# Optimization experiments

Hardware: AMD Instinct MI355X
Metric: run time of the kernel (lower is better)

Reference implementation:

```python
import jax, jax.numpy as jnp
import numpy as np

# dims: M=MC samples, B=graphs, K=latent, H=decoder hidden, N=max nodes, P=permutations
M, B, K, H, N, F_DIM, P = 4, 256, 64, 1024, 50, 3, 64
E = N * (N - 1) // 2  # reduced adjacency = strictly lower triangle
COEFF_A = 1.0
BETA = 1.0
TRIL_I, TRIL_J = np.tril_indices(N, -1)


def setup_inputs() -> dict:
    key = jax.random.key(0)
    ks = jax.random.split(key, 12)
    mean = 0.5 * jax.random.normal(ks[0], (B, K), dtype=jnp.float32)
    logvar = 0.1 * jax.random.normal(ks[1], (B, K), dtype=jnp.float32)
    eps = jax.random.normal(ks[2], (M, B, K), dtype=jnp.float32)
    W1 = jax.random.normal(ks[3], (K, H), dtype=jnp.float32) / np.sqrt(K)
    b1 = jnp.zeros((H,), jnp.float32)
    WA = jax.random.normal(ks[4], (H, E), dtype=jnp.float32) / np.sqrt(H)
    bA = jnp.zeros((E,), jnp.float32)
    WF = jax.random.normal(ks[5], (H, N * F_DIM), dtype=jnp.float32) / np.sqrt(H)
    bF = jnp.zeros((N * F_DIM,), jnp.float32)
    # symmetric binary adjacency with zero diagonal
    U = jax.random.bernoulli(ks[6], 0.15, (B, N, N)).astype(jnp.float32)
    Au = jnp.triu(U, 1)
    A_in = Au + jnp.swapaxes(Au, -1, -2)
    # two bernoulli attributes + one one-hot-categorical attribute (over nodes)
    fb = jax.random.bernoulli(ks[7], 0.3, (B, N, 2)).astype(jnp.float32)
    idx = jax.random.randint(ks[8], (B,), 0, N)
    oh = jax.nn.one_hot(idx, N, dtype=jnp.float32)  # (B, N)
    Fx = jnp.concatenate([fb, oh[..., None]], axis=-1)  # (B, N, 3)
    coeff_Fx = jnp.ones((F_DIM,), jnp.float32)
    permutations = jax.vmap(lambda k: jax.random.permutation(k, N))(
        jax.random.split(ks[9], P)).astype(jnp.int32)  # (P, N)
    return dict(mean=mean, logvar=logvar, eps=eps, W1=W1, b1=b1, WA=WA, bA=bA,
                WF=WF, bF=bF, A_in=A_in, Fx=Fx, coeff_Fx=coeff_Fx,
                permutations=permutations)


def _bernoulli_logprob(x, logits):
    # sum of elementwise Bernoulli log-prob over last axis
    return jnp.sum(x * jax.nn.log_sigmoid(logits)
                   + (1.0 - x) * jax.nn.log_sigmoid(-logits), axis=-1)


def reference(mean, logvar, eps, W1, b1, WA, bA, WF, bF, A_in, Fx, coeff_Fx,
              permutations):
    # pathwise (reparametrised) latent samples: (M, B, K)
    Z = mean + jnp.exp(0.5 * logvar) * eps
    # MLP decoder
    h = jax.nn.relu(Z @ W1 + b1)                       # (M, B, H)
    logits_A = h @ WA + bA                              # (M, B, E)
    logits_Fx = (h @ WF + bF).reshape(M, B, N, F_DIM)   # (M, B, N, F)
    # permutation-matched adjacency: A_perm[b,p,i,j] = A_in[b, perm[p,i], perm[p,j]]
    A_perm = A_in[:, permutations[:, :, None], permutations[:, None, :]]  # (B,P,N,N)
    A_red = A_perm[..., TRIL_I, TRIL_J].reshape(B * P, E)                 # (B*P, E)
    lA = jnp.repeat(logits_A, P, axis=1)                                  # (M, B*P, E)
    nce_A = _bernoulli_logprob(A_red, lA).mean(axis=0)                    # (B*P,)
    nce_A = nce_A.reshape(B, P).max(axis=1)                               # (B,)
    # attribute log-probs: two bernoulli (sum over nodes), one categorical over nodes
    lp_bern = jnp.sum(
        Fx[..., :2] * jax.nn.log_sigmoid(logits_Fx[..., :2])
        + (1.0 - Fx[..., :2]) * jax.nn.log_sigmoid(-logits_Fx[..., :2]),
        axis=-2)                                                          # (M, B, 2)
    lp_cat = jnp.sum(Fx[..., 2] * jax.nn.log_softmax(logits_Fx[..., 2], axis=-1),
                     axis=-1)                                             # (M, B)
    nce_Fx = jnp.concatenate([lp_bern.mean(0), lp_cat.mean(0)[:, None]], axis=-1)  # (B, F)
    # KL(q(z|x) || N(0, I))
    kld = 0.5 * jnp.sum(jnp.exp(logvar) + mean ** 2 - 1.0 - logvar, axis=-1)  # (B,)
    return COEFF_A * nce_A + nce_Fx @ coeff_Fx - BETA * kld
```

## Files before the change

kernel.cpp:

```cpp
#include <hip/hip_runtime.h>
#include <math.h>

#define MM 4
#define BB 256
#define KK 64
#define HH 1024
#define NN 50
#define EE 1225
#define PP 64
#define CTOT 1375
#define NPAD 1408

typedef short short8 __attribute__((ext_vector_type(8)));
typedef float floatx4 __attribute__((ext_vector_type(4)));
typedef unsigned short ushort;

__device__ __forceinline__ ushort f2bf(float f) {
    union { float f; unsigned u; } v; v.f = f;
    unsigned r = v.u + 0x7fffu + ((v.u >> 16) & 1u);
    return (ushort)(r >> 16);
}

__device__ __forceinline__ float logsigm(float l) {
    return -(fmaxf(l, 0.0f) + log1pf(expf(-fabsf(l))));
}

__device__ __forceinline__ float wsum64(float v) {
    #pragma unroll
    for (int m = 1; m < 64; m <<= 1) v += __shfl_xor(v, m);
    return v;
}
__device__ __forceinline__ float wmax64(float v) {
    #pragma unroll
    for (int m = 1; m < 64; m <<= 1) v = fmaxf(v, __shfl_xor(v, m));
    return v;
}

__global__ __launch_bounds__(256) void kA(const float* __restrict__ mean,
                                          const float* __restrict__ logvar,
                                          const float* __restrict__ eps,
                                          const float* __restrict__ W1,
                                          const float* __restrict__ b1,
                                          const float* __restrict__ WA,
                                          const float* __restrict__ WF,
                                          const float* __restrict__ A,
                                          ushort* __restrict__ hB,
                                          ushort* __restrict__ Wt,
                                          float* __restrict__ Sneg,
                                          int*   __restrict__ edgesG,
                                          int*   __restrict__ cntG,
                                          float* __restrict__ kldG) {
    const int t = threadIdx.x;
    __shared__ float smem[64 * 65];
    __shared__ int cnt;

    if (blockIdx.x < 256) {
        const int b = blockIdx.x;
        float4* z4 = (float4*)smem;
        if (t == 0) cnt = 0;
        if (t < 64) {
            float mv = mean[b * 64 + t];
            float lv = logvar[b * 64 + t];
            float sd = expf(0.5f * lv);
            float4 z;
            z.x = mv + sd * eps[(0 * BB + b) * 64 + t];
            z.y = mv + sd * eps[(1 * BB + b) * 64 + t];
            z.z = mv + sd * eps[(2 * BB + b) * 64 + t];
            z.w = mv + sd * eps[(3 * BB + b) * 64 + t];
            z4[t] = z;
            float term = 0.5f * (expf(lv) + mv * mv - 1.0f - lv);
            term = wsum64(term);
            if (t == 0) kldG[b] = term;
        }
        if (t < 4) Sneg[b * 4 + t] = 0.0f;
        __syncthreads();
        const int j0 = t * 4;
        float acc[4][4] = {};
        #pragma unroll 8
        for (int k = 0; k < 64; k++) {
            float4 w = *(const float4*)&W1[k * HH + j0];
            float4 z = z4[k];
            acc[0][0] += z.x * w.x; acc[0][1] += z.x * w.y; acc[0][2] += z.x * w.z; acc[0][3] += z.x * w.w;
            acc[1][0] += z.y * w.x; acc[1][1] += z.y * w.y; acc[1][2] += z.y * w.z; acc[1][3] += z.y * w.w;
            acc[2][0] += z.z * w.x; acc[2][1] += z.z * w.y; acc[2][2] += z.z * w.z; acc[2][3] += z.z * w.w;
            acc[3][0] += z.w * w.x; acc[3][1] += z.w * w.y; acc[3][2] += z.w * w.z; acc[3][3] += z.w * w.w;
        }
        float4 bb = *(const float4*)&b1[j0];
        #pragma unroll
        for (int m = 0; m < 4; m++) {
            unsigned u0 = ((unsigned)f2bf(fmaxf(acc[m][0] + bb.x, 0.f))) |
                          ((unsigned)f2bf(fmaxf(acc[m][1] + bb.y, 0.f)) << 16);
            unsigned u1 = ((unsigned)f2bf(fmaxf(acc[m][2] + bb.z, 0.f))) |
                          ((unsigned)f2bf(fmaxf(acc[m][3] + bb.w, 0.f)) << 16);
            uint2 u; u.x = u0; u.y = u1;
            *(uint2*)&hB[(b * 4 + m) * HH + j0] = u;
        }
        for (int x = t; x < 2500; x += 256) {
            int i = x / NN, j = x - i * NN;
            if (j < i) {
                float a = A[b * 2500 + x];
                if (a != 0.0f) { int id = atomicAdd(&cnt, 1); edgesG[b * 256 + id] = (i << 8) | j; }
            }
        }
        __syncthreads();
        if (t == 0) cntG[b] = cnt;
    } else {
        const int id = blockIdx.x - 256;
        const int kt = id & 15, nt = id >> 4;
        float* T = smem;
        const int k0 = kt * 64, n0 = nt * 64;
        #pragma unroll
        for (int i = 0; i < 16; i++) {
            int x = i * 256 + t;
            int kk = x >> 6, nn = x & 63;
            int gn = n0 + nn, gk = k0 + kk;
            float v = 0.f;
            if (gn < EE)        v = WA[gk * EE + gn];
            else if (gn < CTOT) v = WF[gk * 150 + (gn - EE)];
            T[kk * 65 + nn] = v;
        }
        __syncthreads();
        #pragma unroll
        for (int i = 0; i < 16; i++) {
            int x = i * 256 + t;
            int nn = x >> 6, kk = x & 63;
            Wt[(n0 + nn) * 1024 + k0 + kk] = f2bf(T[kk * 65 + nn]);
        }
    }
}

__global__ __launch_bounds__(256) void k2(const ushort* __restrict__ hB,
                                          const ushort* __restrict__ Wt,
                                          const float* __restrict__ bA,
                                          const float* __restrict__ bF,
                                          float* __restrict__ Lbar,
                                          float* __restrict__ Sneg,
                                          float* __restrict__ lgF) {
    const int ct = blockIdx.x;
    const int rt = blockIdx.y;
    const int t = threadIdx.x;
    const int w = t >> 6, lane = t & 63;
    const int wm = w >> 1, wn = w & 1;
    const int quad = lane >> 4, l16 = lane & 15;
    __shared__ short As[64][72];
    __shared__ short Bs[64][72];
    floatx4 acc[2][2] = {};
    const int row0 = rt * 64, col0 = ct * 64;

    const int r0 = t >> 3, koA = (t & 7) * 8;
    const int r1 = r0 + 32;
    const ushort* pA0 = hB + (row0 + r0) * 1024 + koA;
    const ushort* pA1 = hB + (row0 + r1) * 1024 + koA;
    const ushort* pB0 = Wt + (col0 + r0) * 1024 + koA;
    const ushort* pB1 = Wt + (col0 + r1) * 1024 + koA;

    short8 ra[2], rb[2];
    ra[0] = *(const short8*)(pA0);
    ra[1] = *(const short8*)(pA1);
    rb[0] = *(const short8*)(pB0);
    rb[1] = *(const short8*)(pB1);

    for (int ch = 0; ch < 16; ch++) {
        __syncthreads();
        *(short8*)&As[r0][koA] = ra[0];
        *(short8*)&As[r1][koA] = ra[1];
        *(short8*)&Bs[r0][koA] = rb[0];
        *(short8*)&Bs[r1][koA] = rb[1];
        __syncthreads();
        if (ch < 15) {
            const int off = (ch + 1) * 64;
            ra[0] = *(const short8*)(pA0 + off);
            ra[1] = *(const short8*)(pA1 + off);
            rb[0] = *(const short8*)(pB0 + off);
            rb[1] = *(const short8*)(pB1 + off);
        }
        #pragma unroll
        for (int kk = 0; kk < 2; kk++) {
            int ko = kk * 32 + quad * 8;
            short8 a0 = *(const short8*)&As[wm * 32 + l16][ko];
            short8 a1 = *(const short8*)&As[wm * 32 + 16 + l16][ko];
            short8 b0 = *(const short8*)&Bs[wn * 32 + l16][ko];
            short8 b1 = *(const short8*)&Bs[wn * 32 + 16 + l16][ko];
            acc[0][0] = __builtin_amdgcn_mfma_f32_16x16x32_bf16(a0, b0, acc[0][0], 0, 0, 0);
            acc[0][1] = __builtin_amdgcn_mfma_f32_16x16x32_bf16(a0, b1, acc[0][1], 0, 0, 0);
            acc[1][0] = __builtin_amdgcn_mfma_f32_16x16x32_bf16(a1, b0, acc[1][0], 0, 0, 0);
            acc[1][1] = __builtin_amdgcn_mfma_f32_16x16x32_bf16(a1, b1, acc[1][1], 0, 0, 0);
        }
    }

    #pragma unroll
    for (int mi = 0; mi < 2; mi++) {
        const int grow = row0 + wm * 32 + mi * 16 + quad * 4;
        const int b = grow >> 2;
        float sn0 = 0.f, sn1 = 0.f, sn2 = 0.f, sn3 = 0.f;
        #pragma unroll
        for (int ni = 0; ni < 2; ni++) {
            int gc = col0 + wn * 32 + ni * 16 + l16;
            floatx4 a = acc[mi][ni];
            if (gc < EE) {
                float bias = bA[gc];
                float l0 = a[0] + bias, l1 = a[1] + bias, l2 = a[2] + bias, l3 = a[3] + bias;
                Lbar[b * EE + gc] = 0.25f * (l0 + l1 + l2 + l3);
                sn0 += logsigm(l0); sn1 += logsigm(l1); sn2 += logsigm(l2); sn3 += logsigm(l3);
            } else if (gc < CTOT) {
                int c2 = gc - EE;
                float bias = bF[c2];
                lgF[(b * 4 + 0) * 150 + c2] = a[0] + bias;
                lgF[(b * 4 + 1) * 150 + c2] = a[1] + bias;
                lgF[(b * 4 + 2) * 150 + c2] = a[2] + bias;
                lgF[(b * 4 + 3) * 150 + c2] = a[3] + bias;
            }
        }
        #pragma unroll
        for (int msk = 1; msk < 16; msk <<= 1) {
            sn0 += __shfl_xor(sn0, msk);
            sn1 += __shfl_xor(sn1, msk);
            sn2 += __shfl_xor(sn2, msk);
            sn3 += __shfl_xor(sn3, msk);
        }
        if (l16 == 0) {
            atomicAdd(&Sneg[b * 4 + 0], sn0);
            atomicAdd(&Sneg[b * 4 + 1], sn1);
            atomicAdd(&Sneg[b * 4 + 2], sn2);
            atomicAdd(&Sneg[b * 4 + 3], sn3);
        }
    }
}

__global__ __launch_bounds__(512) void k4(const float* __restrict__ Fx,
                                          const float* __restrict__ coeff,
                                          const int* __restrict__ perms,
                                          const float* __restrict__ Lbar,
                                          const float* __restrict__ Sneg,
                                          const float* __restrict__ lgF,
                                          const int* __restrict__ edgesG,
                                          const int* __restrict__ cntG,
                                          const float* __restrict__ kldG,
                                          float* __restrict__ out) {
    const int b = blockIdx.x;
    const int t = threadIdx.x;
    const int w = t >> 6, lane = t & 63;
    __shared__ int   ip[PP * NN];
    __shared__ float Lb[EE];
    __shared__ int   edges[256];
    __shared__ float lgfs[600];
    __shared__ float mred[4], wmaxs[8];

    const int ne = cntG[b];
    for (int x = t; x < PP * NN; x += 512) {
        int p = x / NN, i = x - p * NN;
        ip[p * NN + perms[x]] = i;
    }
    for (int x = t; x < EE; x += 512) Lb[x] = Lbar[b * EE + x];
    for (int x = t; x < 600; x += 512) lgfs[x] = lgF[b * 600 + x];
    if (t < ne) edges[t] = edgesG[b * 256 + t];
    __syncthreads();

    if (w < 4) {
        float l0 = 0.f, l1 = 0.f, l2 = -INFINITY, x0 = 0.f, x1 = 0.f, x2 = 0.f;
        bool v = lane < NN;
        if (v) {
            l0 = lgfs[w * 150 + lane * 3 + 0];
            l1 = lgfs[w * 150 + lane * 3 + 1];
            l2 = lgfs[w * 150 + lane * 3 + 2];
            x0 = Fx[b * 150 + lane * 3 + 0];
            x1 = Fx[b * 150 + lane * 3 + 1];
            x2 = Fx[b * 150 + lane * 3 + 2];
        }
        float mx = wmax64(l2);
        float es = v ? expf(l2 - mx) : 0.f;
        es = wsum64(es);
        float lse = mx + logf(es);
        float val = 0.f;
        if (v) {
            val = coeff[0] * (logsigm(l0) + x0 * l0)
                + coeff[1] * (logsigm(l1) + x1 * l1)
                + coeff[2] * (x2 * (l2 - lse));
        }
        val = wsum64(val);
        if (lane == 0) mred[w] = val;
    }
    __syncthreads();

    float lmax = -INFINITY;
    for (int p = w; p < PP; p += 8) {
        const int* ipp = &ip[p * NN];
        float acc = 0.f;
        for (int x = lane; x < ne; x += 64) {
            int ed = edges[x];
            int iu = ipp[ed >> 8], iv = ipp[ed & 255];
            int ii = max(iu, iv), jj = min(iu, iv);
            acc += Lb[ii * (ii - 1) / 2 + jj];
        }
        acc = wsum64(acc);
        lmax = fmaxf(lmax, acc);
    }
    if (lane == 0) wmaxs[w] = lmax;
    __syncthreads();
    if (t == 0) {
        float dmax = wmaxs[0];
        #pragma unroll
        for (int i = 1; i < 8; i++) dmax = fmaxf(dmax, wmaxs[i]);
        float sbar = 0.25f * (Sneg[b * 4 + 0] + Sneg[b * 4 + 1] + Sneg[b * 4 + 2] + Sneg[b * 4 + 3]);
        float fxv  = 0.25f * (mred[0] + mred[1] + mred[2] + mred[3]);
        out[b] = (sbar + dmax) + fxv - kldG[b];
    }
}

extern "C" void kernel_launch(void* const* d_in, const int* in_sizes, int n_in,
                              void* d_out, int out_size, void* d_ws, size_t ws_size,
                              hipStream_t stream) {
    const float* mean   = (const float*)d_in[0];
    const float* logvar = (const float*)d_in[1];
    const float* eps    = (const float*)d_in[2];
    const float* W1     = (const float*)d_in[3];
    const float* b1     = (const float*)d_in[4];
    const float* WA     = (const float*)d_in[5];
    const float* bA     = (const float*)d_in[6];
    const float* WF     = (const float*)d_in[7];
    const float* bF     = (const float*)d_in[8];
    const float* A      = (const float*)d_in[9];
    const float* Fx     = (const float*)d_in[10];
    const float* coeff  = (const float*)d_in[11];
    const int*   perms  = (const int*)d_in[12];
    float* out = (float*)d_out;

    ushort* Wt   = (ushort*)d_ws;
    ushort* hB   = Wt + NPAD * 1024;
    float*  Lbar = (float*)(hB + 1024 * 1024);
    float*  Sneg = Lbar + BB * EE;
    float*  lgF  = Sneg + 1024;
    int*    edgesG = (int*)(lgF + 1024 * 150);
    int*    cntG   = edgesG + 256 * 256;
    float*  kldG   = (float*)(cntG + 256);

    kA<<<dim3(608), dim3(256), 0, stream>>>(mean, logvar, eps, W1, b1, WA, WF, A,
                                            hB, Wt, Sneg, edgesG, cntG, kldG);
    k2<<<dim3(22, 16), dim3(256), 0, stream>>>(hB, Wt, bA, bF, Lbar, Sneg, lgF);
    k4<<<dim3(BB), dim3(512), 0, stream>>>(Fx, coeff, perms, Lbar, Sneg, lgF,
                                           edgesG, cntG, kldG, out);
}
```

Measured before the change: 127.4 us.

## Precompute inverse permutations, use full symmetric logit table, double-buffer GEMM LDS

```diff
diff --git a/kernel.cpp b/kernel.cpp
--- a/kernel.cpp
+++ b/kernel.cpp
@@ -44,12 +44,14 @@
                                           const float* __restrict__ WA,
                                           const float* __restrict__ WF,
                                           const float* __restrict__ A,
+                                          const int*   __restrict__ perms,
                                           ushort* __restrict__ hB,
                                           ushort* __restrict__ Wt,
                                           float* __restrict__ Sneg,
                                           int*   __restrict__ edgesG,
                                           int*   __restrict__ cntG,
-                                          float* __restrict__ kldG) {
+                                          float* __restrict__ kldG,
+                                          int*   __restrict__ ipG) {
     const int t = threadIdx.x;
     __shared__ float smem[64 * 65];
     __shared__ int cnt;
@@ -104,7 +106,7 @@
         }
         __syncthreads();
         if (t == 0) cntG[b] = cnt;
-    } else {
+    } else if (blockIdx.x < 608) {
         const int id = blockIdx.x - 256;
         const int kt = id & 15, nt = id >> 4;
         float* T = smem;
@@ -125,6 +127,12 @@
             int x = i * 256 + t;
             int nn = x >> 6, kk = x & 63;
             Wt[(n0 + nn) * 1024 + k0 + kk] = f2bf(T[kk * 65 + nn]);
+        }
+    } else {
+        const int id = blockIdx.x - 608;
+        for (int x = id * 800 + t; x < (id + 1) * 800; x += 256) {
+            int p = x / NN, i = x - p * NN;
+            ipG[p * 51 + perms[x]] = i;
         }
     }
 }
@@ -142,8 +150,8 @@
     const int w = t >> 6, lane = t & 63;
     const int wm = w >> 1, wn = w & 1;
     const int quad = lane >> 4, l16 = lane & 15;
-    __shared__ short As[64][72];
-    __shared__ short Bs[64][72];
+    __shared__ short As[2][64][72];
+    __shared__ short Bs[2][64][72];
     floatx4 acc[2][2] = {};
     const int row0 = rt * 64, col0 = ct * 64;
 
@@ -154,37 +162,44 @@
     const ushort* pB0 = Wt + (col0 + r0) * 1024 + koA;
     const ushort* pB1 = Wt + (col0 + r1) * 1024 + koA;
 
-    short8 ra[2], rb[2];
-    ra[0] = *(const short8*)(pA0);
-    ra[1] = *(const short8*)(pA1);
-    rb[0] = *(const short8*)(pB0);
-    rb[1] = *(const short8*)(pB1);
-
+    short8 ra0 = *(const short8*)(pA0);
+    short8 ra1 = *(const short8*)(pA1);
+    short8 rb0 = *(const short8*)(pB0);
+    short8 rb1 = *(const short8*)(pB1);
+    *(short8*)&As[0][r0][koA] = ra0;
+    *(short8*)&As[0][r1][koA] = ra1;
+    *(short8*)&Bs[0][r0][koA] = rb0;
+    *(short8*)&Bs[0][r1][koA] = rb1;
+    __syncthreads();
+
+    int cur = 0;
     for (int ch = 0; ch < 16; ch++) {
-        __syncthreads();
-        *(short8*)&As[r0][koA] = ra[0];
-        *(short8*)&As[r1][koA] = ra[1];
-        *(short8*)&Bs[r0][koA] = rb[0];
-        *(short8*)&Bs[r1][koA] = rb[1];
-        __syncthreads();
         if (ch < 15) {
             const int off = (ch + 1) * 64;
-            ra[0] = *(const short8*)(pA0 + off);
-            ra[1] = *(const short8*)(pA1 + off);
-            rb[0] = *(const short8*)(pB0 + off);
-            rb[1] = *(const short8*)(pB1 + off);
+            ra0 = *(const short8*)(pA0 + off);
+            ra1 = *(const short8*)(pA1 + off);
+            rb0 = *(const short8*)(pB0 + off);
+            rb1 = *(const short8*)(pB1 + off);
         }
         #pragma unroll
         for (int kk = 0; kk < 2; kk++) {
             int ko = kk * 32 + quad * 8;
-            short8 a0 = *(const short8*)&As[wm * 32 + l16][ko];
-            short8 a1 = *(const short8*)&As[wm * 32 + 16 + l16][ko];
-            short8 b0 = *(const short8*)&Bs[wn * 32 + l16][ko];
-            short8 b1 = *(const short8*)&Bs[wn * 32 + 16 + l16][ko];
+            short8 a0 = *(const short8*)&As[cur][wm * 32 + l16][ko];
+            short8 a1 = *(const short8*)&As[cur][wm * 32 + 16 + l16][ko];
+            short8 b0 = *(const short8*)&Bs[cur][wn * 32 + l16][ko];
+            short8 b1 = *(const short8*)&Bs[cur][wn * 32 + 16 + l16][ko];
             acc[0][0] = __builtin_amdgcn_mfma_f32_16x16x32_bf16(a0, b0, acc[0][0], 0, 0, 0);
             acc[0][1] = __builtin_amdgcn_mfma_f32_16x16x32_bf16(a0, b1, acc[0][1], 0, 0, 0);
             acc[1][0] = __builtin_amdgcn_mfma_f32_16x16x32_bf16(a1, b0, acc[1][0], 0, 0, 0);
             acc[1][1] = __builtin_amdgcn_mfma_f32_16x16x32_bf16(a1, b1, acc[1][1], 0, 0, 0);
+        }
+        if (ch < 15) {
+            *(short8*)&As[cur ^ 1][r0][koA] = ra0;
+            *(short8*)&As[cur ^ 1][r1][koA] = ra1;
+            *(short8*)&Bs[cur ^ 1][r0][koA] = rb0;
+            *(short8*)&Bs[cur ^ 1][r1][koA] = rb1;
+            __syncthreads();
+            cur ^= 1;
         }
     }
 
@@ -229,7 +244,7 @@
 
 __global__ __launch_bounds__(512) void k4(const float* __restrict__ Fx,
                                           const float* __restrict__ coeff,
-                                          const int* __restrict__ perms,
+                                          const int* __restrict__ ipG,
                                           const float* __restrict__ Lbar,
                                           const float* __restrict__ Sneg,
                                           const float* __restrict__ lgF,
@@ -240,21 +255,38 @@
     const int b = blockIdx.x;
     const int t = threadIdx.x;
     const int w = t >> 6, lane = t & 63;
-    __shared__ int   ip[PP * NN];
-    __shared__ float Lb[EE];
+    __shared__ int   ip[PP * 51];
+    __shared__ float LbF[NN * 51];
     __shared__ int   edges[256];
     __shared__ float lgfs[600];
-    __shared__ float mred[4], wmaxs[8];
+    __shared__ float mred[4];
+    __shared__ float psum[8][64];
 
     const int ne = cntG[b];
-    for (int x = t; x < PP * NN; x += 512) {
-        int p = x / NN, i = x - p * NN;
-        ip[p * NN + perms[x]] = i;
-    }
-    for (int x = t; x < EE; x += 512) Lb[x] = Lbar[b * EE + x];
+    for (int x = t; x < PP * 51; x += 512) ip[x] = ipG[x];
+    for (int x = t; x < 2500; x += 512) {
+        int i = x / NN, j = x - i * NN;
+        if (j < i) {
+            float v = Lbar[b * EE + i * (i - 1) / 2 + j];
+            LbF[i * 51 + j] = v;
+            LbF[j * 51 + i] = v;
+        }
+    }
     for (int x = t; x < 600; x += 512) lgfs[x] = lgF[b * 600 + x];
     if (t < ne) edges[t] = edgesG[b * 256 + t];
     __syncthreads();
+
+    {
+        const int ipB = lane * 51;
+        float acc = 0.f;
+        for (int x = w; x < ne; x += 8) {
+            int ed = edges[x];
+            int iu = ip[ipB + (ed >> 8)];
+            int iv = ip[ipB + (ed & 255)];
+            acc += LbF[iu * 51 + iv];
+        }
+        psum[w][lane] = acc;
+    }
 
     if (w < 4) {
         float l0 = 0.f, l1 = 0.f, l2 = -INFINITY, x0 = 0.f, x1 = 0.f, x2 = 0.f;
@@ -282,28 +314,16 @@
     }
     __syncthreads();
 
-    float lmax = -INFINITY;
-    for (int p = w; p < PP; p += 8) {
-        const int* ipp = &ip[p * NN];
-        float acc = 0.f;
-        for (int x = lane; x < ne; x += 64) {
-            int ed = edges[x];
-            int iu = ipp[ed >> 8], iv = ipp[ed & 255];
-            int ii = max(iu, iv), jj = min(iu, iv);
-            acc += Lb[ii * (ii - 1) / 2 + jj];
-        }
-        acc = wsum64(acc);
-        lmax = fmaxf(lmax, acc);
-    }
-    if (lane == 0) wmaxs[w] = lmax;
-    __syncthreads();
-    if (t == 0) {
-        float dmax = wmaxs[0];
-        #pragma unroll
-        for (int i = 1; i < 8; i++) dmax = fmaxf(dmax, wmaxs[i]);
-        float sbar = 0.25f * (Sneg[b * 4 + 0] + Sneg[b * 4 + 1] + Sneg[b * 4 + 2] + Sneg[b * 4 + 3]);
-        float fxv  = 0.25f * (mred[0] + mred[1] + mred[2] + mred[3]);
-        out[b] = (sbar + dmax) + fxv - kldG[b];
+    if (w == 0) {
+        float s = psum[0][lane];
+        #pragma unroll
+        for (int i = 1; i < 8; i++) s += psum[i][lane];
+        float dmax = wmax64(s);
+        if (lane == 0) {
+            float sbar = 0.25f * (Sneg[b * 4 + 0] + Sneg[b * 4 + 1] + Sneg[b * 4 + 2] + Sneg[b * 4 + 3]);
+            float fxv  = 0.25f * (mred[0] + mred[1] + mred[2] + mred[3]);
+            out[b] = (sbar + dmax) + fxv - kldG[b];
+        }
     }
 }
 
@@ -333,10 +353,11 @@
     int*    edgesG = (int*)(lgF + 1024 * 150);
     int*    cntG   = edgesG + 256 * 256;
     float*  kldG   = (float*)(cntG + 256);
-
-    kA<<<dim3(608), dim3(256), 0, stream>>>(mean, logvar, eps, W1, b1, WA, WF, A,
-                                            hB, Wt, Sneg, edgesG, cntG, kldG);
+    int*    ipG    = (int*)(kldG + 256);
+
+    kA<<<dim3(612), dim3(256), 0, stream>>>(mean, logvar, eps, W1, b1, WA, WF, A, perms,
+                                            hB, Wt, Sneg, edgesG, cntG, kldG, ipG);
     k2<<<dim3(22, 16), dim3(256), 0, stream>>>(hB, Wt, bA, bF, Lbar, Sneg, lgF);
-    k4<<<dim3(BB), dim3(512), 0, stream>>>(Fx, coeff, perms, Lbar, Sneg, lgF,
+    k4<<<dim3(BB), dim3(512), 0, stream>>>(Fx, coeff, ipG, Lbar, Sneg, lgF,
                                            edgesG, cntG, kldG, out);
 }
```

Result: no change. 125.4 us (-1.5%).
